# Performance work log

Hardware: AMD Instinct MI355X
Metric: run time of the kernel (lower is better)

The kernel has to match this reference:

```python
import jax, jax.numpy as jnp
import numpy as np

B, S = 8, 2048
E1, E2, E3 = 256, 256, 512
E = E1 + E2 + E3
NEG_SLOPE = 0.2


def setup_inputs() -> dict:
    key = jax.random.key(0)
    ks = jax.random.split(key, 11)
    scale = 1.0 / np.sqrt(E)
    return {
        "embeding1": jax.random.normal(ks[0], (B, S, E1), jnp.float32),
        "embeding2": jax.random.normal(ks[1], (B, S, E2), jnp.float32),
        "embeding3": jax.random.normal(ks[2], (B, S, E3), jnp.float32),
        # nn.Linear weights are [out, in]; apply as x @ W.T + b
        "Wq": jax.random.uniform(ks[3], (E, E), jnp.float32, -scale, scale),
        "bq": jax.random.uniform(ks[4], (E,), jnp.float32, -scale, scale),
        "Wk": jax.random.uniform(ks[5], (E, E), jnp.float32, -scale, scale),
        "bk": jax.random.uniform(ks[6], (E,), jnp.float32, -scale, scale),
        "Wv": jax.random.uniform(ks[7], (E, E), jnp.float32, -scale, scale),
        "bv": jax.random.uniform(ks[8], (E,), jnp.float32, -scale, scale),
        "Wf": jax.random.uniform(ks[9], (E, E), jnp.float32, -scale, scale),
        "bf": jax.random.uniform(ks[10], (E,), jnp.float32, -scale, scale),
    }


def reference(embeding1, embeding2, embeding3, Wq, bq, Wk, bk, Wv, bv, Wf, bf):
    x = jnp.concatenate([embeding1, embeding2, embeding3], axis=-1)  # [B,S,E]
    q = jnp.einsum("bse,oe->bso", x, Wq) + bq
    k = jnp.einsum("bse,oe->bso", x, Wk) + bk
    v = jnp.einsum("bse,oe->bso", x, Wv) + bv
    # NOTE: no 1/sqrt(d) scaling, faithful to the original module
    scores = jnp.einsum("bqe,bke->bqk", q, k)  # [B,S,S]
    probs = jax.nn.softmax(scores, axis=-1)
    weighted = jnp.einsum("bqk,bke->bqe", probs, v)  # [B,S,E]
    out = jnp.einsum("bse,oe->bso", weighted, Wf) + bf
    return jnp.where(out >= 0, out, NEG_SLOPE * out)
```

## Files before the change

kernel.cpp:

```cpp
#include <hip/hip_runtime.h>
#include <hip/hip_fp16.h>

typedef _Float16 half8 __attribute__((ext_vector_type(8)));
typedef _Float16 half4v __attribute__((ext_vector_type(4)));
typedef float floatx4 __attribute__((ext_vector_type(4)));

__device__ __forceinline__ void load_lds16(const void* g, void* l) {
    __builtin_amdgcn_global_load_lds(
        (const __attribute__((address_space(1))) void*)g,
        (__attribute__((address_space(3))) void*)l,
        16, 0, 0);
}

__device__ __forceinline__ void stage_half(const _Float16* g, long ld, _Float16* dst) {
    const int t = threadIdx.x;
#pragma unroll
    for (int j = 0; j < 2; ++j) {
        const int c = j * 512 + t;
        const int row = c >> 3;
        const int slot = (c & 7) ^ (row & 7);
        load_lds16(g + (long)row * ld + slot * 8, dst + c * 8);
    }
}

#define GEMM_PRELUDE                                                               \
    const int lane = threadIdx.x & 63;                                             \
    const int w    = threadIdx.x >> 6;                                             \
    const int wr   = w >> 2;                                                       \
    const int wc   = w & 3;                                                        \
    const int rsel = lane & 15, gsel = lane >> 4;                                  \
    const int NT = K >> 6;                                                         \
    (void)lane;
#define STAGE(BUF, KT)                                                             \
    stage_half(A + (KT) * 64, lda, lds + (BUF) * 32768);                           \
    stage_half(A + (long)128 * lda + (KT) * 64, lda, lds + (BUF) * 32768 + 8192);  \
    stage_half(B + (KT) * 64, ldb, lds + (BUF) * 32768 + 16384);                   \
    stage_half(B + (long)128 * ldb + (KT) * 64, ldb, lds + (BUF) * 32768 + 24576);
#define READ_A(dst, AH, MH)                                                        \
    _Pragma("unroll") for (int mi = 0; mi < 4; ++mi) {                             \
        const int r = ((MH) * 4 + mi) * 16 + rsel;                                 \
        dst[mi][0] = *(const half8*)&(AH)[r * 64 + ((gsel ^ (r & 7)) << 3)];       \
        dst[mi][1] = *(const half8*)&(AH)[r * 64 + (((4 + gsel) ^ (r & 7)) << 3)]; \
    }
#define READ_B(dst, BH, NH)                                                        \
    _Pragma("unroll") for (int ni = 0; ni < 2; ++ni) {                             \
        const int rn = (wc & 1) * 64 + ((NH) * 2 + ni) * 16 + rsel;                \
        dst[ni][0] = *(const half8*)&(BH)[rn * 64 + ((gsel ^ (rn & 7)) << 3)];     \
        dst[ni][1] = *(const half8*)&(BH)[rn * 64 + (((4 + gsel) ^ (rn & 7)) << 3)]; \
    }
#define MFMA_Q(MH, NH, A_, B_)                                                     \
    _Pragma("unroll") for (int mi = 0; mi < 4; ++mi)                               \
    _Pragma("unroll") for (int ni = 0; ni < 2; ++ni) {                             \
        acc[(MH) * 4 + mi][(NH) * 2 + ni] = __builtin_amdgcn_mfma_f32_16x16x32_f16( \
            A_[mi][0], B_[ni][0], acc[(MH) * 4 + mi][(NH) * 2 + ni], 0, 0, 0);     \
        acc[(MH) * 4 + mi][(NH) * 2 + ni] = __builtin_amdgcn_mfma_f32_16x16x32_f16( \
            A_[mi][1], B_[ni][1], acc[(MH) * 4 + mi][(NH) * 2 + ni], 0, 0, 0);     \
    }
#define SB0 __builtin_amdgcn_sched_barrier(0)

__device__ __forceinline__ void gemm256_core(const _Float16* A, long lda,
                                             const _Float16* B, long ldb,
                                             int K, floatx4 acc[8][4],
                                             _Float16* lds) {
    GEMM_PRELUDE
    half8 a_lo[4][2], a_hi[4][2], b_lo[2][2], b_hi[2][2];
    STAGE(0, 0);
    asm volatile("s_waitcnt vmcnt(0)" ::: "memory");
    __builtin_amdgcn_s_barrier();
    SB0;
#pragma unroll 1
    for (int t = 0; t < NT; ++t) {
        const int buf = t & 1;
        if (t + 1 < NT) { STAGE(buf ^ 1, t + 1); }
        const _Float16* Ah = lds + buf * 32768 + wr * 8192;
        const _Float16* Bh = lds + buf * 32768 + 16384 + (wc >> 1) * 8192;
        READ_A(a_lo, Ah, 0);
        READ_B(b_lo, Bh, 0);
        SB0;
        READ_A(a_hi, Ah, 1);
        SB0;
        READ_B(b_hi, Bh, 1);
        asm volatile("s_waitcnt lgkmcnt(12)" ::: "memory");
        SB0;
        MFMA_Q(0, 0, a_lo, b_lo);
        asm volatile("s_waitcnt lgkmcnt(4)" ::: "memory");
        SB0;
        MFMA_Q(1, 0, a_hi, b_lo);
        asm volatile("s_waitcnt lgkmcnt(0)" ::: "memory");
        SB0;
        MFMA_Q(0, 1, a_lo, b_hi);
        MFMA_Q(1, 1, a_hi, b_hi);
        asm volatile("s_waitcnt vmcnt(0)" ::: "memory");
        __builtin_amdgcn_s_barrier();
        SB0;
    }
}

__device__ __forceinline__ void gemm256_core_pv(const _Float16* A, long lda,
                                                const _Float16* B, long ldb,
                                                int K, floatx4 acc[8][4],
                                                _Float16* lds, const float* scl) {
    GEMM_PRELUDE
    half8 a_lo[4][2], a_hi[4][2], b_lo[2][2], b_hi[2][2];
    STAGE(0, 0);
    asm volatile("s_waitcnt vmcnt(0)" ::: "memory");
    __builtin_amdgcn_s_barrier();
    SB0;
#pragma unroll 1
    for (int t = 0; t < NT; ++t) {
        const int buf = t & 1;
        if (t + 1 < NT) { STAGE(buf ^ 1, t + 1); }
        const _Float16* Ah = lds + buf * 32768 + wr * 8192;
        const _Float16* Bh = lds + buf * 32768 + 16384 + (wc >> 1) * 8192;
        const float* srow = scl + (t >> 2) * 256 + wr * 128 + rsel;
        float s_lo[4], s_hi[4];
#pragma unroll
        for (int mi = 0; mi < 4; ++mi) s_lo[mi] = srow[mi * 16];
#pragma unroll
        for (int mi = 0; mi < 4; ++mi) s_hi[mi] = srow[64 + mi * 16];
        SB0;
        READ_A(a_lo, Ah, 0);
        READ_B(b_lo, Bh, 0);
        SB0;
        READ_A(a_hi, Ah, 1);
        SB0;
        READ_B(b_hi, Bh, 1);
        asm volatile("s_waitcnt lgkmcnt(12)" ::: "memory");
        SB0;
#pragma unroll
        for (int mi = 0; mi < 4; ++mi) {
            const _Float16 h = (_Float16)s_lo[mi];
            a_lo[mi][0] = a_lo[mi][0] * h;
            a_lo[mi][1] = a_lo[mi][1] * h;
        }
        MFMA_Q(0, 0, a_lo, b_lo);
        asm volatile("s_waitcnt lgkmcnt(4)" ::: "memory");
        SB0;
#pragma unroll
        for (int mi = 0; mi < 4; ++mi) {
            const _Float16 h = (_Float16)s_hi[mi];
            a_hi[mi][0] = a_hi[mi][0] * h;
            a_hi[mi][1] = a_hi[mi][1] * h;
        }
        MFMA_Q(1, 0, a_hi, b_lo);
        asm volatile("s_waitcnt lgkmcnt(0)" ::: "memory");
        SB0;
        MFMA_Q(0, 1, a_lo, b_hi);
        MFMA_Q(1, 1, a_hi, b_hi);
        asm volatile("s_waitcnt vmcnt(0)" ::: "memory");
        __builtin_amdgcn_s_barrier();
        SB0;
    }
}

__device__ __forceinline__ void zero_acc8(floatx4 acc[8][4]) {
    const floatx4 z = {0.f, 0.f, 0.f, 0.f};
#pragma unroll
    for (int m = 0; m < 8; ++m)
#pragma unroll
        for (int n = 0; n < 4; ++n) acc[m][n] = z;
}


__global__ __launch_bounds__(256) void prep_kernel(const float* e1, const float* e2,
                                                   const float* e3, const float* Wq,
                                                   const float* Wk, const float* Wv,
                                                   const float* Wf, _Float16* X,
                                                   _Float16* Wdst) {
    const int bid = blockIdx.x;
    if (bid < 16384) {
        long i = ((long)bid * 256 + threadIdx.x) * 4;
        int m = (int)(i >> 10);
        int c = (int)(i & 1023);
        const float* src;
        if (c < 256)      src = e1 + (long)m * 256 + c;
        else if (c < 512) src = e2 + (long)m * 256 + (c - 256);
        else              src = e3 + (long)m * 512 + (c - 512);
        float4 f = *(const float4*)src;
        half4v h;
        h[0] = (_Float16)f.x; h[1] = (_Float16)f.y;
        h[2] = (_Float16)f.z; h[3] = (_Float16)f.w;
        *(half4v*)&X[i] = h;
    } else {
        long i = ((long)(bid - 16384) * 256 + threadIdx.x) * 4;
        int which = (int)(i >> 20);
        long off = i & 1048575;
        const float* w = which == 0 ? Wq : which == 1 ? Wk : which == 2 ? Wv : Wf;
        float4 f = *(const float4*)(w + off);
        half4v h;
        h[0] = (_Float16)f.x; h[1] = (_Float16)f.y;
        h[2] = (_Float16)f.z; h[3] = (_Float16)f.w;
        *(half4v*)&Wdst[i] = h;
    }
}

__global__ __launch_bounds__(512, 2) void qkv_kernel(const _Float16* X, const _Float16* W,
                                                     const float* bq, const float* bk,
                                                     const float* bv, _Float16* q,
                                                     _Float16* k, _Float16* vT) {
    extern __shared__ _Float16 lds[];
    const int m0 = blockIdx.x * 256;
    const int n0 = blockIdx.y * 256;
    const int z  = blockIdx.z;
    floatx4 acc[8][4];
    zero_acc8(acc);
    gemm256_core(X + (long)m0 * 1024, 1024,
                 W + (long)z * 1048576 + (long)n0 * 1024, 1024, 1024, acc, lds);

    const float* bias = (z == 0) ? bq : (z == 1) ? bk : bv;
    const int lane = threadIdx.x & 63;
    const int w = threadIdx.x >> 6;
    const int wr = w >> 2, wc = w & 3;
    const int rsel = lane & 15, gsel = lane >> 4;

    if (z == 2) {
        const int rb = wr * 128 + gsel * 4;
        const int cb = wc * 64 + rsel;
#pragma unroll
        for (int mI = 0; mI < 8; ++mI) {
#pragma unroll
            for (int nI = 0; nI < 4; ++nI) {
                const int c = cb + nI * 16;
                const int r = rb + mI * 16;
                const float bb = bias[n0 + c];
                half4v vv;
#pragma unroll
                for (int j = 0; j < 4; ++j) vv[j] = (_Float16)(acc[mI][nI][j] + bb);
                *(half4v*)&lds[c * 256 + (r ^ ((c & 7) << 3))] = vv;
            }
        }
        __syncthreads();
#pragma unroll
        for (int it = 0; it < 16; ++it) {
            const int idx = it * 512 + threadIdx.x;
            const int c = idx >> 5;
            const int mc = idx & 31;
            half8 v = *(const half8*)&lds[c * 256 + ((mc * 8) ^ ((c & 7) << 3))];
            *(half8*)&vT[(long)(n0 + c) * 16384 + m0 + mc * 8] = v;
        }
    } else {
        _Float16* dst = (z == 0) ? q : k;
        const int r0 = m0 + wr * 128 + gsel * 4;
        const int c0 = n0 + wc * 64 + rsel;
#pragma unroll
        for (int mI = 0; mI < 8; ++mI) {
#pragma unroll
            for (int nI = 0; nI < 4; ++nI) {
                const int r = r0 + mI * 16;
                const int c = c0 + nI * 16;
                const float bb = bias[c];
#pragma unroll
                for (int j = 0; j < 4; ++j)
                    dst[(long)(r + j) * 1024 + c] = (_Float16)(acc[mI][nI][j] + bb);
            }
        }
    }
}

__global__ __launch_bounds__(512, 2) void scores_kernel(const _Float16* qh,
                                                        const _Float16* kh,
                                                        _Float16* es, float* tmax,
                                                        float* tsum) {
    extern __shared__ _Float16 lds[];
    const int b = blockIdx.x;
    const int m0 = (blockIdx.y >> 3) * 256;
    const int tile = blockIdx.y & 7;
    const int n0 = tile * 256;
    floatx4 acc[8][4];
    zero_acc8(acc);
    gemm256_core(qh + ((long)b * 2048 + m0) * 1024, 1024,
                 kh + ((long)b * 2048 + n0) * 1024, 1024, 1024, acc, lds);

    const int lane = threadIdx.x & 63;
    const int w = threadIdx.x >> 6;
    const int wr = w >> 2, wc = w & 3;
    const int rsel = lane & 15, gsel = lane >> 4;
    float* red  = (float*)lds;
    float* red2 = (float*)lds + 1024;

#pragma unroll
    for (int m = 0; m < 8; ++m) {
#pragma unroll
        for (int j = 0; j < 4; ++j) {
            float v = acc[m][0][j];
#pragma unroll
            for (int n = 1; n < 4; ++n) v = fmaxf(v, acc[m][n][j]);
#pragma unroll
            for (int d = 1; d < 16; d <<= 1) v = fmaxf(v, __shfl_xor(v, d));
            if (rsel == 0) red[(wr * 128 + m * 16 + gsel * 4 + j) * 4 + wc] = v;
        }
    }
    __syncthreads();

#pragma unroll
    for (int m = 0; m < 8; ++m) {
#pragma unroll
        for (int j = 0; j < 4; ++j) {
            const int row = wr * 128 + m * 16 + gsel * 4 + j;
            float4 rv = *(const float4*)&red[row * 4];
            const float mxv = fmaxf(fmaxf(rv.x, rv.y), fmaxf(rv.z, rv.w));
            float s = 0.f;
#pragma unroll
            for (int n = 0; n < 4; ++n) {
                float e = __expf(acc[m][n][j] - mxv);
                acc[m][n][j] = e;
                s += e;
            }
#pragma unroll
            for (int d = 1; d < 16; d <<= 1) s += __shfl_xor(s, d);
            if (rsel == 0) red2[row * 4 + wc] = s;
        }
    }
    __syncthreads();

    if (wc == 0 && rsel == 0) {
        const long base = ((long)b * 8 + tile) * 2048 + m0;
#pragma unroll
        for (int m = 0; m < 8; ++m) {
#pragma unroll
            for (int j = 0; j < 4; ++j) {
                const int row = wr * 128 + m * 16 + gsel * 4 + j;
                float4 rv = *(const float4*)&red[row * 4];
                float4 sv = *(const float4*)&red2[row * 4];
                tmax[base + row] = fmaxf(fmaxf(rv.x, rv.y), fmaxf(rv.z, rv.w));
                tsum[base + row] = sv.x + sv.y + sv.z + sv.w;
            }
        }
    }
    __syncthreads();

#pragma unroll
    for (int m = 0; m < 8; ++m) {
        const int r = wr * 128 + m * 16 + gsel * 4;
#pragma unroll
        for (int n = 0; n < 4; ++n) {
            const int c = wc * 64 + n * 16 + rsel;
            const int s = (c & 7) ^ ((c >> 3) & 7);
            half4v hv;
#pragma unroll
            for (int j = 0; j < 4; ++j) hv[j] = (_Float16)acc[m][n][j];
            *(half4v*)&lds[c * 256 + (r ^ (s << 3))] = hv;
        }
    }
    __syncthreads();
    const long rbase = (long)b * 2048 * 2048;
#pragma unroll
    for (int it = 0; it < 16; ++it) {
        const int idx = it * 512 + threadIdx.x;
        const int r = idx >> 5;
        const int chunk = idx & 31;
        half8 h;
#pragma unroll
        for (int e = 0; e < 8; ++e) {
            const int c = chunk * 8 + e;
            const int s = e ^ (chunk & 7);
            h[e] = lds[c * 256 + (r ^ (s << 3))];
        }
        *(half8*)&es[rbase + (long)(m0 + r) * 2048 + n0 + chunk * 8] = h;
    }
}

__global__ __launch_bounds__(512, 2) void pv_kernel(const _Float16* es,
                                                    const _Float16* vT,
                                                    const float* tmax,
                                                    const float* tsum,
                                                    _Float16* wt) {
    extern __shared__ _Float16 lds[];
    const int batch = blockIdx.x;
    const int m0 = (blockIdx.y >> 2) * 256;
    const int n0 = (blockIdx.y & 3) * 256;
    float* scl = (float*)(lds + 65536);
    if (threadIdx.x < 256) {
        const int row = m0 + threadIdx.x;
        float m[8];
        float mg = -1e30f;
#pragma unroll
        for (int t = 0; t < 8; ++t) {
            m[t] = tmax[((long)batch * 8 + t) * 2048 + row];
            mg = fmaxf(mg, m[t]);
        }
        float Z = 0.f;
#pragma unroll
        for (int t = 0; t < 8; ++t)
            Z += tsum[((long)batch * 8 + t) * 2048 + row] * __expf(m[t] - mg);
        const float inv = 1.0f / Z;
#pragma unroll
        for (int t = 0; t < 8; ++t)
            scl[t * 256 + threadIdx.x] = __expf(m[t] - mg) * inv;
    }
    __syncthreads();
    floatx4 acc[8][4];
    zero_acc8(acc);
    gemm256_core_pv(es + ((long)batch * 2048 + m0) * 2048, 2048,
                    vT + (long)n0 * 16384 + (long)batch * 2048, 16384, 2048, acc,
                    lds, scl);

    const int lane = threadIdx.x & 63;
    const int w = threadIdx.x >> 6;
    const int wr = w >> 2, wc = w & 3;
    const int r0 = wr * 128 + (lane >> 4) * 4;
    const int c0 = n0 + wc * 64 + (lane & 15);
#pragma unroll
    for (int m = 0; m < 8; ++m) {
#pragma unroll
        for (int n = 0; n < 4; ++n) {
            const int r = r0 + m * 16;
            const int c = c0 + n * 16;
#pragma unroll
            for (int j = 0; j < 4; ++j)
                wt[((long)batch * 2048 + m0 + r + j) * 1024 + c] =
                    (_Float16)acc[m][n][j];
        }
    }
}

__global__ __launch_bounds__(512, 2) void out_kernel(const _Float16* wt, const _Float16* Wf,
                                                     const float* bf_, float* out) {
    extern __shared__ _Float16 lds[];
    const int m0 = blockIdx.x * 256;
    const int n0 = blockIdx.y * 256;
    floatx4 acc[8][4];
    zero_acc8(acc);
    gemm256_core(wt + (long)m0 * 1024, 1024, Wf + (long)n0 * 1024, 1024, 1024, acc, lds);

    const int lane = threadIdx.x & 63;
    const int w = threadIdx.x >> 6;
    const int wr = w >> 2, wc = w & 3;
    const int r0 = m0 + wr * 128 + (lane >> 4) * 4;
    const int c0 = n0 + wc * 64 + (lane & 15);
#pragma unroll
    for (int m = 0; m < 8; ++m) {
#pragma unroll
        for (int n = 0; n < 4; ++n) {
            const int r = r0 + m * 16;
            const int c = c0 + n * 16;
            const float bb = bf_[c];
#pragma unroll
            for (int j = 0; j < 4; ++j) {
                float y = acc[m][n][j] + bb;
                y = (y >= 0.f) ? y : 0.2f * y;
                out[(long)(r + j) * 1024 + c] = y;
            }
        }
    }
}

extern "C" void kernel_launch(void* const* d_in, const int* in_sizes, int n_in,
                              void* d_out, int out_size, void* d_ws, size_t ws_size,
                              hipStream_t stream) {
    const float* e1 = (const float*)d_in[0];
    const float* e2 = (const float*)d_in[1];
    const float* e3 = (const float*)d_in[2];
    const float* Wq = (const float*)d_in[3];
    const float* bq = (const float*)d_in[4];
    const float* Wk = (const float*)d_in[5];
    const float* bk = (const float*)d_in[6];
    const float* Wv = (const float*)d_in[7];
    const float* bv = (const float*)d_in[8];
    const float* Wf = (const float*)d_in[9];
    const float* bf_ = (const float*)d_in[10];
    float* out = (float*)d_out;

    const int LDS_BYTES = 131072;
    const int LDS_PV = 131072 + 8192;
    (void)hipFuncSetAttribute((const void*)qkv_kernel,
                              hipFuncAttributeMaxDynamicSharedMemorySize, LDS_BYTES);
    (void)hipFuncSetAttribute((const void*)scores_kernel,
                              hipFuncAttributeMaxDynamicSharedMemorySize, LDS_BYTES);
    (void)hipFuncSetAttribute((const void*)pv_kernel,
                              hipFuncAttributeMaxDynamicSharedMemorySize, LDS_PV);
    (void)hipFuncSetAttribute((const void*)out_kernel,
                              hipFuncAttributeMaxDynamicSharedMemorySize, LDS_BYTES);

    char* ws = (char*)d_ws;
    const size_t MB = 1024 * 1024;
    _Float16* Xh    = (_Float16*)(ws + 0);
    _Float16* Wh    = (_Float16*)(ws + 32 * MB);
    _Float16* qh    = (_Float16*)(ws + 40 * MB);
    _Float16* kh    = (_Float16*)(ws + 72 * MB);
    _Float16* vT    = (_Float16*)(ws + 104 * MB);
    _Float16* wt    = (_Float16*)(ws + 136 * MB);
    _Float16* es    = (_Float16*)(ws + 168 * MB);
    float* tmax     = (float*)(ws + 232 * MB);
    float* tsum     = (float*)(ws + 232 * MB + 524288);

    prep_kernel<<<20480, 256, 0, stream>>>(e1, e2, e3, Wq, Wk, Wv, Wf, Xh, Wh);
    qkv_kernel<<<dim3(64, 4, 3), 512, LDS_BYTES, stream>>>(Xh, Wh, bq, bk, bv, qh, kh, vT);
    scores_kernel<<<dim3(8, 64), 512, LDS_BYTES, stream>>>(qh, kh, es, tmax, tsum);
    pv_kernel<<<dim3(8, 32), 512, LDS_PV, stream>>>(es, vT, tmax, tsum, wt);
    out_kernel<<<dim3(64, 4), 512, LDS_BYTES, stream>>>(wt, Wh + 3 * 1048576, bf_, out);
}
```

Measured before the change: 313.2 us.

## Restructure scores epilogue: LDS partial row reductions and row-major two-pass store

Replaces the 16-lane shuffle reductions for row max and row sum with per-thread partials written to a padded LDS buffer, then reduced by 256 threads, one per row. The transposed LDS staging with scalar half gathers is replaced by a row-major swizzled layout that allows vectorized half8 LDS reads. The 256-row tile is written out in two halves to fit the staging buffer. This cuts shuffle and scalar-LDS instruction overhead in the epilogue, at the cost of extra LDS (136 KB dynamic) and more barriers. The larger LDS request may affect how many blocks fit per CU.

```diff
diff --git a/kernel.cpp b/kernel.cpp
--- a/kernel.cpp
+++ b/kernel.cpp
@@ -275,30 +275,42 @@
     const int w = threadIdx.x >> 6;
     const int wr = w >> 2, wc = w & 3;
     const int rsel = lane & 15, gsel = lane >> 4;
-    float* red  = (float*)lds;
-    float* red2 = (float*)lds + 1024;
-
-#pragma unroll
-    for (int m = 0; m < 8; ++m) {
-#pragma unroll
-        for (int j = 0; j < 4; ++j) {
-            float v = acc[m][0][j];
-#pragma unroll
-            for (int n = 1; n < 4; ++n) v = fmaxf(v, acc[m][n][j]);
-#pragma unroll
-            for (int d = 1; d < 16; d <<= 1) v = fmaxf(v, __shfl_xor(v, d));
-            if (rsel == 0) red[(wr * 128 + m * 16 + gsel * 4 + j) * 4 + wc] = v;
-        }
-    }
-    __syncthreads();
+    const int tid = threadIdx.x;
+    float* redp   = (float*)(lds + 32768);
+    float* rowmax = (float*)(lds + 67584);
+    const int slot = wc * 16 + rsel;
 
 #pragma unroll
     for (int m = 0; m < 8; ++m) {
 #pragma unroll
         for (int j = 0; j < 4; ++j) {
             const int row = wr * 128 + m * 16 + gsel * 4 + j;
-            float4 rv = *(const float4*)&red[row * 4];
-            const float mxv = fmaxf(fmaxf(rv.x, rv.y), fmaxf(rv.z, rv.w));
+            float v = acc[m][0][j];
+#pragma unroll
+            for (int n = 1; n < 4; ++n) v = fmaxf(v, acc[m][n][j]);
+            redp[row * 68 + slot] = v;
+        }
+    }
+    __syncthreads();
+
+    if (tid < 256) {
+        const float* rr = redp + tid * 68;
+        float mv = -1e30f;
+#pragma unroll
+        for (int q4 = 0; q4 < 16; ++q4) {
+            float4 f = ((const float4*)rr)[q4];
+            mv = fmaxf(mv, fmaxf(fmaxf(f.x, f.y), fmaxf(f.z, f.w)));
+        }
+        rowmax[tid] = mv;
+    }
+    __syncthreads();
+
+#pragma unroll
+    for (int m = 0; m < 8; ++m) {
+#pragma unroll
+        for (int j = 0; j < 4; ++j) {
+            const int row = wr * 128 + m * 16 + gsel * 4 + j;
+            const float mxv = rowmax[row];
             float s = 0.f;
 #pragma unroll
             for (int n = 0; n < 4; ++n) {
@@ -306,57 +318,70 @@
                 acc[m][n][j] = e;
                 s += e;
             }
-#pragma unroll
-            for (int d = 1; d < 16; d <<= 1) s += __shfl_xor(s, d);
-            if (rsel == 0) red2[row * 4 + wc] = s;
+            redp[row * 68 + slot] = s;
+        }
+    }
+#pragma unroll
+    for (int m = 0; m < 4; ++m) {
+#pragma unroll
+        for (int j = 0; j < 4; ++j) {
+            const int lr = wr * 64 + m * 16 + gsel * 4 + j;
+            const int g = lr & 7;
+#pragma unroll
+            for (int n = 0; n < 4; ++n) {
+                const int c = wc * 64 + n * 16 + rsel;
+                lds[lr * 256 + (c ^ (g << 3))] = (_Float16)acc[m][n][j];
+            }
         }
     }
     __syncthreads();
 
-    if (wc == 0 && rsel == 0) {
+    if (tid < 256) {
+        const float* rr = redp + tid * 68;
+        float sv = 0.f;
+#pragma unroll
+        for (int q4 = 0; q4 < 16; ++q4) {
+            float4 f = ((const float4*)rr)[q4];
+            sv += f.x + f.y + f.z + f.w;
+        }
         const long base = ((long)b * 8 + tile) * 2048 + m0;
-#pragma unroll
-        for (int m = 0; m < 8; ++m) {
-#pragma unroll
-            for (int j = 0; j < 4; ++j) {
-                const int row = wr * 128 + m * 16 + gsel * 4 + j;
-                float4 rv = *(const float4*)&red[row * 4];
-                float4 sv = *(const float4*)&red2[row * 4];
-                tmax[base + row] = fmaxf(fmaxf(rv.x, rv.y), fmaxf(rv.z, rv.w));
-                tsum[base + row] = sv.x + sv.y + sv.z + sv.w;
+        tmax[base + tid] = rowmax[tid];
+        tsum[base + tid] = sv;
+    }
+    const long rbase = (long)b * 2048 * 2048;
+#pragma unroll
+    for (int it = 0; it < 8; ++it) {
+        const int idx = it * 512 + tid;
+        const int lr = idx >> 5;
+        const int chunk = idx & 31;
+        half8 v = *(const half8*)&lds[lr * 256 + ((chunk ^ (lr & 7)) * 8)];
+        const int rg = (lr & 63) + ((lr >> 6) << 7);
+        *(half8*)&es[rbase + (long)(m0 + rg) * 2048 + n0 + chunk * 8] = v;
+    }
+    __syncthreads();
+
+#pragma unroll
+    for (int m = 4; m < 8; ++m) {
+#pragma unroll
+        for (int j = 0; j < 4; ++j) {
+            const int lr = wr * 64 + (m - 4) * 16 + gsel * 4 + j;
+            const int g = lr & 7;
+#pragma unroll
+            for (int n = 0; n < 4; ++n) {
+                const int c = wc * 64 + n * 16 + rsel;
+                lds[lr * 256 + (c ^ (g << 3))] = (_Float16)acc[m][n][j];
             }
         }
     }
     __syncthreads();
-
-#pragma unroll
-    for (int m = 0; m < 8; ++m) {
-        const int r = wr * 128 + m * 16 + gsel * 4;
-#pragma unroll
-        for (int n = 0; n < 4; ++n) {
-            const int c = wc * 64 + n * 16 + rsel;
-            const int s = (c & 7) ^ ((c >> 3) & 7);
-            half4v hv;
-#pragma unroll
-            for (int j = 0; j < 4; ++j) hv[j] = (_Float16)acc[m][n][j];
-            *(half4v*)&lds[c * 256 + (r ^ (s << 3))] = hv;
-        }
-    }
-    __syncthreads();
-    const long rbase = (long)b * 2048 * 2048;
-#pragma unroll
-    for (int it = 0; it < 16; ++it) {
-        const int idx = it * 512 + threadIdx.x;
-        const int r = idx >> 5;
+#pragma unroll
+    for (int it = 0; it < 8; ++it) {
+        const int idx = it * 512 + tid;
+        const int lr = idx >> 5;
         const int chunk = idx & 31;
-        half8 h;
-#pragma unroll
-        for (int e = 0; e < 8; ++e) {
-            const int c = chunk * 8 + e;
-            const int s = e ^ (chunk & 7);
-            h[e] = lds[c * 256 + (r ^ (s << 3))];
-        }
-        *(half8*)&es[rbase + (long)(m0 + r) * 2048 + n0 + chunk * 8] = h;
+        half8 v = *(const half8*)&lds[lr * 256 + ((chunk ^ (lr & 7)) * 8)];
+        const int rg = 64 + (lr & 63) + ((lr >> 6) << 7);
+        *(half8*)&es[rbase + (long)(m0 + rg) * 2048 + n0 + chunk * 8] = v;
     }
 }
 
@@ -462,11 +487,12 @@
     float* out = (float*)d_out;
 
     const int LDS_BYTES = 131072;
+    const int LDS_SC = 136192;
     const int LDS_PV = 131072 + 8192;
     (void)hipFuncSetAttribute((const void*)qkv_kernel,
                               hipFuncAttributeMaxDynamicSharedMemorySize, LDS_BYTES);
     (void)hipFuncSetAttribute((const void*)scores_kernel,
-                              hipFuncAttributeMaxDynamicSharedMemorySize, LDS_BYTES);
+                              hipFuncAttributeMaxDynamicSharedMemorySize, LDS_SC);
     (void)hipFuncSetAttribute((const void*)pv_kernel,
                               hipFuncAttributeMaxDynamicSharedMemorySize, LDS_PV);
     (void)hipFuncSetAttribute((const void*)out_kernel,
@@ -486,7 +512,7 @@
 
     prep_kernel<<<20480, 256, 0, stream>>>(e1, e2, e3, Wq, Wk, Wv, Wf, Xh, Wh);
     qkv_kernel<<<dim3(64, 4, 3), 512, LDS_BYTES, stream>>>(Xh, Wh, bq, bk, bv, qh, kh, vT);
-    scores_kernel<<<dim3(8, 64), 512, LDS_BYTES, stream>>>(qh, kh, es, tmax, tsum);
+    scores_kernel<<<dim3(8, 64), 512, LDS_SC, stream>>>(qh, kh, es, tmax, tsum);
     pv_kernel<<<dim3(8, 32), 512, LDS_PV, stream>>>(es, vT, tmax, tsum, wt);
     out_kernel<<<dim3(64, 4), 512, LDS_BYTES, stream>>>(wt, Wh + 3 * 1048576, bf_, out);
 }
```

Result: faster. 296.1 us, median of 2 (-5.5%).
